# Optimization experiments

Measured on AMD Instinct MI355X. Metric: run time of the kernel, lower is better.

Reference implementation:

```python
import jax, jax.numpy as jnp
import numpy as np

B, H, W, C = 64, 56, 56, 192
NH, WS, SS = 6, 7, 3
N = WS * WS
MLP_H = 4 * C
HD = C // NH
NW = (H // WS) * (W // WS)
EPS = 1e-5


def _rel_pos_index():
    coords = np.stack(np.meshgrid(np.arange(WS), np.arange(WS), indexing='ij')).reshape(2, -1)
    rel = (coords[:, :, None] - coords[:, None, :]).transpose(1, 2, 0)
    rel[..., 0] += WS - 1
    rel[..., 1] += WS - 1
    rel[..., 0] *= 2 * WS - 1
    return rel.sum(-1)  # [N, N]


def _attn_mask():
    img = np.zeros((H, W))
    cnt = 0
    sl = (slice(0, -WS), slice(-WS, -SS), slice(-SS, None))
    for hs in sl:
        for ws in sl:
            img[hs, ws] = cnt
            cnt += 1
    mw = img.reshape(H // WS, WS, W // WS, WS).transpose(0, 2, 1, 3).reshape(-1, N)
    am = mw[:, None, :] - mw[:, :, None]
    return np.where(am != 0, -100.0, 0.0).astype(np.float32)  # [nW, N, N]


REL_IDX = jnp.asarray(_rel_pos_index())
ATTN_MASK = jnp.asarray(_attn_mask())


def _ln(x, g, b):
    m = x.mean(-1, keepdims=True)
    v = x.var(-1, keepdims=True)
    return (x - m) / jnp.sqrt(v + EPS) * g + b


def setup_inputs() -> dict:
    key = jax.random.key(0)
    ks = jax.random.split(key, 16)
    p = lambda k, shape: jax.random.normal(k, shape, dtype=jnp.float32) * 0.02
    return {
        'x': jax.random.normal(ks[0], (B, H * W, C), dtype=jnp.float32),
        'norm1_g': jnp.ones((C,), jnp.float32),
        'norm1_b': jnp.zeros((C,), jnp.float32),
        'qkv_w': p(ks[1], (3 * C, C)),
        'qkv_b': jnp.zeros((3 * C,), jnp.float32),
        'rpb': p(ks[2], ((2 * WS - 1) * (2 * WS - 1), NH)),
        'gate': jnp.full((NH,), 0.001, jnp.float32),
        'proj_w': p(ks[3], (C, C)),
        'proj_b': jnp.zeros((C,), jnp.float32),
        'norm2_g': jnp.ones((C,), jnp.float32),
        'norm2_b': jnp.zeros((C,), jnp.float32),
        'fc1_w': p(ks[4], (MLP_H, C)),
        'fc1_b': jnp.zeros((MLP_H,), jnp.float32),
        'bn_g': jnp.ones((MLP_H,), jnp.float32),
        'bn_b': jnp.zeros((MLP_H,), jnp.float32),
        'fc2_w': p(ks[5], (C, MLP_H)),
        'fc2_b': jnp.zeros((C,), jnp.float32),
    }


def reference(x, norm1_g, norm1_b, qkv_w, qkv_b, rpb, gate, proj_w, proj_b,
              norm2_g, norm2_b, fc1_w, fc1_b, bn_g, bn_b, fc2_w, fc2_b):
    shortcut = x  # [B, L, C]
    y = _ln(x, norm1_g, norm1_b).reshape(B, H, W, C)
    # cyclic shift
    y = jnp.roll(y, (-SS, -SS), axis=(1, 2))
    # window partition -> [B*nW, N, C]
    yw = y.reshape(B, H // WS, WS, W // WS, WS, C).transpose(0, 1, 3, 2, 4, 5).reshape(-1, N, C)
    qkv = (yw @ qkv_w.T + qkv_b).reshape(-1, N, 3, NH, HD).transpose(2, 0, 3, 1, 4)
    q, k, v = qkv[0], qkv[1], qkv[2]  # [B_, NH, N, HD]
    scale = HD ** (-0.5)
    attn = jnp.einsum('bhnd,bhmd->bhnm', q * scale, k)  # [B_, NH, N, N]
    bias = rpb[REL_IDX].transpose(2, 0, 1)  # [NH, N, N]
    attn = attn + bias[None]
    attn = attn.reshape(B, NW, NH, N, N) + ATTN_MASK[None, :, None]
    attn = jax.nn.softmax(attn.reshape(-1, NH, N, N), axis=-1)
    attn = attn * jax.nn.sigmoid(gate).reshape(1, NH, 1, 1)  # post-softmax gate
    o = jnp.einsum('bhnm,bhmd->bhnd', attn, v).transpose(0, 2, 1, 3).reshape(-1, N, C)
    o = o @ proj_w.T + proj_b
    # window reverse + reverse shift
    o = o.reshape(B, H // WS, W // WS, WS, WS, C).transpose(0, 1, 3, 2, 4, 5).reshape(B, H, W, C)
    o = jnp.roll(o, (SS, SS), axis=(1, 2)).reshape(B, H * W, C)
    x = shortcut + o
    # MLP with eval-mode BatchNorm1d (running_mean=0, running_var=1)
    z = _ln(x, norm2_g, norm2_b)
    z = z @ fc1_w.T + fc1_b
    z = z / jnp.sqrt(1.0 + EPS) * bn_g + bn_b
    z = jax.nn.gelu(z, approximate=False)
    z = z @ fc2_w.T + fc2_b
    return x + z
```

## Files before the change

kernel.cpp:

```cpp
#include <hip/hip_runtime.h>
#include <hip/hip_bf16.h>
#include <math.h>


typedef __attribute__((ext_vector_type(8))) short short8;
typedef __attribute__((ext_vector_type(4))) short short4v;
typedef __attribute__((ext_vector_type(4))) float floatx4;

static __device__ __forceinline__ float bf2f(__hip_bfloat16 v) { return __bfloat162float(v); }

static __device__ __forceinline__ short f2bs(float f) {
    union { __hip_bfloat16 h; short s; } u;
    u.h = __float2bfloat16(f);
    return u.s;
}

__global__ __launch_bounds__(256)
void cvt_w(const float* __restrict__ a, const float* __restrict__ b,
           const float* __restrict__ c, const float* __restrict__ d,
           __hip_bfloat16* __restrict__ o)
{
    int i = blockIdx.x * 256 + threadIdx.x;
    float v;
    if (i < 110592)      v = a[i];
    else if (i < 147456) v = b[i - 110592];
    else if (i < 294912) v = c[i - 147456];
    else                 v = d[i - 294912];
    o[i] = __float2bfloat16(v);
}

__global__ __launch_bounds__(256)
void ln1_shift_win(const float* __restrict__ x,
                   const float* __restrict__ g,
                   const float* __restrict__ bt,
                   __hip_bfloat16* __restrict__ yw)
{
    int r = blockIdx.x * 4 + (threadIdx.x >> 6);
    int lane = threadIdx.x & 63;
    int win = r / 49, t = r - win * 49;
    int b = win >> 6, wi = win & 63;
    int wh = wi >> 3, ww = wi & 7;
    int tr = t / 7, tc = t - tr * 7;
    int hs = wh * 7 + tr + 3; if (hs >= 56) hs -= 56;
    int ws = ww * 7 + tc + 3; if (ws >= 56) ws -= 56;
    const float* src = x + ((size_t)b * 3136 + hs * 56 + ws) * 192;
    float v0 = src[lane];
    float v1 = src[lane + 64];
    float v2 = src[lane + 128];
    float s  = v0 + v1 + v2;
    float s2 = v0 * v0 + v1 * v1 + v2 * v2;
#pragma unroll
    for (int off = 32; off; off >>= 1) { s += __shfl_xor(s, off); s2 += __shfl_xor(s2, off); }
    float mean = s * (1.0f / 192.0f);
    float var  = s2 * (1.0f / 192.0f) - mean * mean;
    float rstd = rsqrtf(var + 1e-5f);
    __hip_bfloat16* dst = yw + (size_t)r * 192;
    dst[lane]       = __float2bfloat16((v0 - mean) * rstd * g[lane]       + bt[lane]);
    dst[lane + 64]  = __float2bfloat16((v1 - mean) * rstd * g[lane + 64]  + bt[lane + 64]);
    dst[lane + 128] = __float2bfloat16((v2 - mean) * rstd * g[lane + 128] + bt[lane + 128]);
}

__global__ __launch_bounds__(256)
void ln2_kernel(const float* __restrict__ x1,
                const float* __restrict__ g,
                const float* __restrict__ bt,
                __hip_bfloat16* __restrict__ z)
{
    int r = blockIdx.x * 4 + (threadIdx.x >> 6);
    int lane = threadIdx.x & 63;
    const float* src = x1 + (size_t)r * 192;
    float v0 = src[lane];
    float v1 = src[lane + 64];
    float v2 = src[lane + 128];
    float s  = v0 + v1 + v2;
    float s2 = v0 * v0 + v1 * v1 + v2 * v2;
#pragma unroll
    for (int off = 32; off; off >>= 1) { s += __shfl_xor(s, off); s2 += __shfl_xor(s2, off); }
    float mean = s * (1.0f / 192.0f);
    float var  = s2 * (1.0f / 192.0f) - mean * mean;
    float rstd = rsqrtf(var + 1e-5f);
    __hip_bfloat16* dst = z + (size_t)r * 192;
    dst[lane]       = __float2bfloat16((v0 - mean) * rstd * g[lane]       + bt[lane]);
    dst[lane + 64]  = __float2bfloat16((v1 - mean) * rstd * g[lane + 64]  + bt[lane + 64]);
    dst[lane + 128] = __float2bfloat16((v2 - mean) * rstd * g[lane + 128] + bt[lane + 128]);
}

__global__ __launch_bounds__(256)
void build_tbl(const float* __restrict__ rpb, float* __restrict__ tbl)
{
    int bid = blockIdx.x;
    int head = bid >> 2, cls = bid & 3;
    int ch = cls >> 1, cw = cls & 1;
    for (int idx = threadIdx.x; idx < 4096; idx += 256) {
        int tile = idx >> 8, lane = (idx >> 2) & 63, rg = idx & 3;
        int mt = tile >> 2, nt = tile & 3;
        int lm = lane & 15, quad = lane >> 4;
        int i = nt * 16 + lm;
        int j = mt * 16 + quad * 4 + rg;
        float v;
        if (i >= 49 || j >= 49) {
            v = -1e30f;
        } else {
            int ri = i / 7, ci = i - ri * 7;
            int rj = j / 7, cj = j - rj * 7;
            int bidx = (ri - rj + 6) * 13 + (ci - cj + 6);
            v = rpb[bidx * 6 + head];
            int rio = ch ? (ri < 4 ? 1 : 2) : 0;
            int cio = cw ? (ci < 4 ? 1 : 2) : 0;
            int rjo = ch ? (rj < 4 ? 1 : 2) : 0;
            int cjo = cw ? (cj < 4 ? 1 : 2) : 0;
            if (rio * 3 + cio != rjo * 3 + cjo) v -= 100.0f;
        }
        tbl[(size_t)bid * 4096 + idx] = v;
    }
}

__global__ __launch_bounds__(256)
void attn_mfma(const __hip_bfloat16* __restrict__ qkv,
               const float* __restrict__ tbl,
               const float* __restrict__ gate,
               __hip_bfloat16* __restrict__ o)
{
    __shared__ __align__(16) char lds[49152];
    const int wave = threadIdx.x >> 6, lane = threadIdx.x & 63;
    const int lm = lane & 15, quad = lane >> 4;
    const int idx = blockIdx.x * 4 + wave;
    const int win = idx / 6;
    const int head = idx - win * 6;
    const int wi = win & 63;
    const int cls = (((wi >> 3) == 7) ? 2 : 0) + (((wi & 7) == 7) ? 1 : 0);

    char* vTb = lds + wave * 12288;
    char* Pb  = vTb + 4096;

    const __hip_bfloat16* base = qkv + (size_t)win * 49 * 576 + head * 32;

    {
        short8 v0 = {0,0,0,0,0,0,0,0}, v1 = {0,0,0,0,0,0,0,0};
        short8 v2 = {0,0,0,0,0,0,0,0}, v3 = {0,0,0,0,0,0,0,0};
        if (lane < 49) {
            const short* p = (const short*)(base + 384) + (size_t)lane * 576;
            v0 = *(const short8*)(p);
            v1 = *(const short8*)(p + 8);
            v2 = *(const short8*)(p + 16);
            v3 = *(const short8*)(p + 24);
        }
#pragma unroll
        for (int d = 0; d < 32; ++d) {
            short val = (d < 8) ? v0[d & 7] : (d < 16) ? v1[d & 7] : (d < 24) ? v2[d & 7] : v3[d & 7];
            *(short*)(vTb + ((d * 128 + lane * 2) ^ ((d & 7) << 4))) = val;
        }
    }

    short8 qf[4], kf[4];
    const short* qsrc = (const short*)base + quad * 8;
    const short* ksrc = (const short*)(base + 192) + quad * 8;
#pragma unroll
    for (int tt = 0; tt < 4; ++tt) {
        int t = tt * 16 + lm;
        if (t < 49) {
            qf[tt] = *(const short8*)(qsrc + (size_t)t * 576);
            kf[tt] = *(const short8*)(ksrc + (size_t)t * 576);
        } else {
            qf[tt] = (short8){0,0,0,0,0,0,0,0};
            kf[tt] = (short8){0,0,0,0,0,0,0,0};
        }
    }

    const floatx4 z4 = {0.f, 0.f, 0.f, 0.f};
    floatx4 s[4][4];
#pragma unroll
    for (int mt = 0; mt < 4; ++mt)
#pragma unroll
        for (int nt = 0; nt < 4; ++nt)
            s[mt][nt] = __builtin_amdgcn_mfma_f32_16x16x32_bf16(kf[mt], qf[nt], z4, 0, 0, 0);

    const float* tb = tbl + (size_t)(head * 4 + cls) * 4096 + lane * 4;
#pragma unroll
    for (int mt = 0; mt < 4; ++mt)
#pragma unroll
        for (int nt = 0; nt < 4; ++nt) {
            floatx4 b = *(const floatx4*)(tb + (mt * 4 + nt) * 256);
#pragma unroll
            for (int rg = 0; rg < 4; ++rg)
                s[mt][nt][rg] = s[mt][nt][rg] * 0.17677669529663689f + b[rg];
        }

    const float gt = 1.0f / (1.0f + __expf(-gate[head]));

    float inv[4];
#pragma unroll
    for (int nt = 0; nt < 4; ++nt) {
        float mx = -1e30f;
#pragma unroll
        for (int mt = 0; mt < 4; ++mt)
#pragma unroll
            for (int rg = 0; rg < 4; ++rg) mx = fmaxf(mx, s[mt][nt][rg]);
        mx = fmaxf(mx, __shfl_xor(mx, 16));
        mx = fmaxf(mx, __shfl_xor(mx, 32));
        float sum = 0.f;
#pragma unroll
        for (int mt = 0; mt < 4; ++mt)
#pragma unroll
            for (int rg = 0; rg < 4; ++rg) {
                float e = __expf(s[mt][nt][rg] - mx);
                s[mt][nt][rg] = e;
                sum += e;
            }
        sum += __shfl_xor(sum, 16);
        sum += __shfl_xor(sum, 32);
        inv[nt] = gt / sum;
    }

#pragma unroll
    for (int nt = 0; nt < 4; ++nt) {
        int row = nt * 16 + lm;
#pragma unroll
        for (int mt = 0; mt < 4; ++mt) {
            short4v pk = { f2bs(s[mt][nt][0] * inv[nt]), f2bs(s[mt][nt][1] * inv[nt]),
                           f2bs(s[mt][nt][2] * inv[nt]), f2bs(s[mt][nt][3] * inv[nt]) };
            int off = (row * 128 + mt * 32 + quad * 8) ^ ((row & 7) << 4);
            *(short4v*)(Pb + off) = pk;
        }
    }

    floatx4 oacc[4][2];
#pragma unroll
    for (int pt = 0; pt < 4; ++pt)
#pragma unroll
        for (int nt = 0; nt < 2; ++nt) oacc[pt][nt] = z4;

#pragma unroll
    for (int ks = 0; ks < 2; ++ks) {
        short8 vfr[2];
#pragma unroll
        for (int nt = 0; nt < 2; ++nt) {
            int row = nt * 16 + lm;
            vfr[nt] = *(const short8*)(vTb + ((row * 128 + ks * 64 + quad * 16) ^ ((row & 7) << 4)));
        }
#pragma unroll
        for (int pt = 0; pt < 4; ++pt) {
            int row = pt * 16 + lm;
            short8 pfr = *(const short8*)(Pb + ((row * 128 + ks * 64 + quad * 16) ^ ((row & 7) << 4)));
#pragma unroll
            for (int nt = 0; nt < 2; ++nt)
                oacc[pt][nt] = __builtin_amdgcn_mfma_f32_16x16x32_bf16(pfr, vfr[nt], oacc[pt][nt], 0, 0, 0);
        }
    }

    __hip_bfloat16* obase = o + (size_t)win * 49 * 192 + head * 32;
#pragma unroll
    for (int pt = 0; pt < 4; ++pt) {
#pragma unroll
        for (int rg = 0; rg < 4; ++rg) {
            int q = pt * 16 + quad * 4 + rg;
            if (q < 49) {
#pragma unroll
                for (int nt = 0; nt < 2; ++nt)
                    obase[(size_t)q * 192 + nt * 16 + lm] = __float2bfloat16(oacc[pt][nt][rg]);
            }
        }
    }
}

template <int MODE>
__global__ __launch_bounds__(256, 2)
void gemm_bt(const __hip_bfloat16* __restrict__ A,
             const __hip_bfloat16* __restrict__ W,
             const float* __restrict__ bias,
             const float* __restrict__ ex0,
             const float* __restrict__ ex1,
             void* __restrict__ OutV,
             int K, int Ncols)
{
    __shared__ __align__(16) char lds[(128 * 32 + 64 * 32) * 2];
    short* sA = (short*)lds;
    short* sB = (short*)(lds + 8192);

    const int tid  = threadIdx.x;
    const int wave = tid >> 6, lane = tid & 63;
    const int m0 = blockIdx.x * 128;
    const int n0 = blockIdx.y * 64;
    const int wm = wave >> 1, wn = wave & 1;
    const int lm = lane & 15, quad = lane >> 4;

    floatx4 acc[4][2];
#pragma unroll
    for (int mt = 0; mt < 4; ++mt)
#pragma unroll
        for (int nt = 0; nt < 2; ++nt) acc[mt][nt] = (floatx4){0.f, 0.f, 0.f, 0.f};

    for (int kk = 0; kk < K; kk += 32) {
#pragma unroll
        for (int i = 0; i < 2; ++i) {
            int c = i * 256 + tid;
            int row = c >> 2, kc = c & 3;
            const __hip_bfloat16* gp = A + (size_t)(m0 + row) * K + kk + kc * 8;
            char* lp = lds + (i * 256 + wave * 64) * 16;
            __builtin_amdgcn_global_load_lds((const __attribute__((address_space(1))) void*)gp,
                                             (__attribute__((address_space(3))) void*)lp, 16, 0, 0);
        }
        {
            int c = tid;
            int row = c >> 2, kc = c & 3;
            const __hip_bfloat16* gp = W + (size_t)(n0 + row) * K + kk + kc * 8;
            char* lp = lds + 8192 + (wave * 64) * 16;
            __builtin_amdgcn_global_load_lds((const __attribute__((address_space(1))) void*)gp,
                                             (__attribute__((address_space(3))) void*)lp, 16, 0, 0);
        }
        asm volatile("s_waitcnt vmcnt(0)" ::: "memory");
        __syncthreads();

        short8 af[4], bf[2];
#pragma unroll
        for (int mt = 0; mt < 4; ++mt)
            af[mt] = *(const short8*)(sA + ((wm * 64 + mt * 16 + lm) * 32 + quad * 8));
#pragma unroll
        for (int nt = 0; nt < 2; ++nt)
            bf[nt] = *(const short8*)(sB + ((wn * 32 + nt * 16 + lm) * 32 + quad * 8));
#pragma unroll
        for (int mt = 0; mt < 4; ++mt)
#pragma unroll
            for (int nt = 0; nt < 2; ++nt)
                acc[mt][nt] = __builtin_amdgcn_mfma_f32_16x16x32_bf16(af[mt], bf[nt], acc[mt][nt], 0, 0, 0);
        __syncthreads();
    }

#pragma unroll
    for (int mt = 0; mt < 4; ++mt) {
#pragma unroll
        for (int nt = 0; nt < 2; ++nt) {
            int col = n0 + wn * 32 + nt * 16 + lm;
            float bcol = bias[col];
#pragma unroll
            for (int rg = 0; rg < 4; ++rg) {
                int row = m0 + wm * 64 + mt * 16 + quad * 4 + rg;
                float val = acc[mt][nt][rg] + bcol;
                if (MODE == 0) {
                    ((__hip_bfloat16*)OutV)[(size_t)row * Ncols + col] = __float2bfloat16(val);
                } else if (MODE == 1) {
                    int win = row / 49, t = row - win * 49;
                    int b = win >> 6, wi = win & 63;
                    int wh = wi >> 3, ww = wi & 7;
                    int tr = t / 7, tc = t - tr * 7;
                    int h = wh * 7 + tr + 3; if (h >= 56) h -= 56;
                    int w = ww * 7 + tc + 3; if (w >= 56) w -= 56;
                    size_t dst = ((size_t)b * 3136 + h * 56 + w) * 192 + col;
                    ((float*)OutV)[dst] = val + ex0[dst];
                } else if (MODE == 2) {
                    float t2 = val * (ex0[col] * 0.99999500003749968f) + ex1[col];
                    float ge = 0.5f * t2 * (1.0f + erff(t2 * 0.70710678118654752f));
                    ((__hip_bfloat16*)OutV)[(size_t)row * Ncols + col] = __float2bfloat16(ge);
                } else {
                    size_t dst = (size_t)row * Ncols + col;
                    ((float*)OutV)[dst] = val + ex0[dst];
                }
            }
        }
    }
}

extern "C" void kernel_launch(void* const* d_in, const int* in_sizes, int n_in,
                              void* d_out, int out_size, void* d_ws, size_t ws_size,
                              hipStream_t stream)
{
    const float* x      = (const float*)d_in[0];
    const float* n1g    = (const float*)d_in[1];
    const float* n1b    = (const float*)d_in[2];
    const float* qkv_w  = (const float*)d_in[3];
    const float* qkv_b  = (const float*)d_in[4];
    const float* rpb    = (const float*)d_in[5];
    const float* gate   = (const float*)d_in[6];
    const float* proj_w = (const float*)d_in[7];
    const float* proj_b = (const float*)d_in[8];
    const float* n2g    = (const float*)d_in[9];
    const float* n2b    = (const float*)d_in[10];
    const float* fc1_w  = (const float*)d_in[11];
    const float* fc1_b  = (const float*)d_in[12];
    const float* bn_g   = (const float*)d_in[13];
    const float* bn_b   = (const float*)d_in[14];
    const float* fc2_w  = (const float*)d_in[15];
    const float* fc2_b  = (const float*)d_in[16];
    float* out = (float*)d_out;

    char* ws = (char*)d_ws;
    const int NCH = (ws_size >= 155025408u) ? 4 : 8;
    const size_t buf1max = (NCH == 4) ? 77070336u : 38535168u;
    __hip_bfloat16* buf0 = (__hip_bfloat16*)(ws);
    __hip_bfloat16* buf1 = (__hip_bfloat16*)(ws + 77070336);
    __hip_bfloat16* wbuf = (__hip_bfloat16*)(ws + 77070336 + buf1max);
    __hip_bfloat16* wq = wbuf;
    __hip_bfloat16* wp = wbuf + 110592;
    __hip_bfloat16* w1 = wbuf + 147456;
    __hip_bfloat16* w2 = wbuf + 294912;

    const int WINS = 4096 / NCH;
    const int ROWS = WINS * 49;
    const int GX   = ROWS / 128;

    float* tbl = (float*)(ws + 77070336 + (size_t)ROWS * 576 * 2);

    cvt_w<<<dim3(1728), 256, 0, stream>>>(qkv_w, proj_w, fc1_w, fc2_w, wbuf);
    build_tbl<<<dim3(24), 256, 0, stream>>>(rpb, tbl);

    ln1_shift_win<<<dim3(200704 / 4), 256, 0, stream>>>(x, n1g, n1b, buf0);

    for (int c = 0; c < NCH; ++c) {
        const __hip_bfloat16* ywc = buf0 + (size_t)c * ROWS * 192;
        __hip_bfloat16*       oc  = buf0 + (size_t)c * ROWS * 192;
        gemm_bt<0><<<dim3(GX, 9), 256, 0, stream>>>(ywc, wq, qkv_b, nullptr, nullptr, buf1, 192, 576);
        attn_mfma<<<dim3(WINS * 6 / 4), 256, 0, stream>>>(buf1, tbl, gate, oc);
    }

    gemm_bt<1><<<dim3(1568, 3), 256, 0, stream>>>(buf0, wp, proj_b, x, nullptr, out, 192, 192);

    ln2_kernel<<<dim3(200704 / 4), 256, 0, stream>>>(out, n2g, n2b, buf0);

    for (int c = 0; c < NCH; ++c) {
        const __hip_bfloat16* zc = buf0 + (size_t)c * ROWS * 192;
        float*                xc = out  + (size_t)c * ROWS * 192;
        gemm_bt<2><<<dim3(GX, 12), 256, 0, stream>>>(zc, w1, fc1_b, bn_g, bn_b, buf1, 192, 768);
        gemm_bt<3><<<dim3(GX, 3), 256, 0, stream>>>(buf1, w2, fc2_b, xc, nullptr, xc, 768, 192);
    }
}
```

Measured before the change: 965.5 us.

## Fuse LayerNorm2, fc1+BN+GELU and fc2 into one MLP kernel

Replaces the ln2 kernel and the chunked fc1/fc2 GEMM launches with a single kernel per 64-row tile. The tile is normalized into LDS, and the 768-wide hidden layer is produced 128 columns at a time into double-buffered LDS, then consumed immediately by fc2 with register accumulators. The aim is to stop writing and re-reading the large hidden activation and the normalized input through global memory, and to cut launch count. In exchange, each block reloads weight fragments straight from global memory without LDS staging, and register pressure is high, which may limit occupancy.

```diff
diff --git a/kernel.cpp b/kernel.cpp
--- a/kernel.cpp
+++ b/kernel.cpp
@@ -55,31 +55,6 @@
     float var  = s2 * (1.0f / 192.0f) - mean * mean;
     float rstd = rsqrtf(var + 1e-5f);
     __hip_bfloat16* dst = yw + (size_t)r * 192;
-    dst[lane]       = __float2bfloat16((v0 - mean) * rstd * g[lane]       + bt[lane]);
-    dst[lane + 64]  = __float2bfloat16((v1 - mean) * rstd * g[lane + 64]  + bt[lane + 64]);
-    dst[lane + 128] = __float2bfloat16((v2 - mean) * rstd * g[lane + 128] + bt[lane + 128]);
-}
-
-__global__ __launch_bounds__(256)
-void ln2_kernel(const float* __restrict__ x1,
-                const float* __restrict__ g,
-                const float* __restrict__ bt,
-                __hip_bfloat16* __restrict__ z)
-{
-    int r = blockIdx.x * 4 + (threadIdx.x >> 6);
-    int lane = threadIdx.x & 63;
-    const float* src = x1 + (size_t)r * 192;
-    float v0 = src[lane];
-    float v1 = src[lane + 64];
-    float v2 = src[lane + 128];
-    float s  = v0 + v1 + v2;
-    float s2 = v0 * v0 + v1 * v1 + v2 * v2;
-#pragma unroll
-    for (int off = 32; off; off >>= 1) { s += __shfl_xor(s, off); s2 += __shfl_xor(s2, off); }
-    float mean = s * (1.0f / 192.0f);
-    float var  = s2 * (1.0f / 192.0f) - mean * mean;
-    float rstd = rsqrtf(var + 1e-5f);
-    __hip_bfloat16* dst = z + (size_t)r * 192;
     dst[lane]       = __float2bfloat16((v0 - mean) * rstd * g[lane]       + bt[lane]);
     dst[lane + 64]  = __float2bfloat16((v1 - mean) * rstd * g[lane + 64]  + bt[lane + 64]);
     dst[lane + 128] = __float2bfloat16((v2 - mean) * rstd * g[lane + 128] + bt[lane + 128]);
@@ -338,7 +313,7 @@
                 float val = acc[mt][nt][rg] + bcol;
                 if (MODE == 0) {
                     ((__hip_bfloat16*)OutV)[(size_t)row * Ncols + col] = __float2bfloat16(val);
-                } else if (MODE == 1) {
+                } else {
                     int win = row / 49, t = row - win * 49;
                     int b = win >> 6, wi = win & 63;
                     int wh = wi >> 3, ww = wi & 7;
@@ -347,14 +322,148 @@
                     int w = ww * 7 + tc + 3; if (w >= 56) w -= 56;
                     size_t dst = ((size_t)b * 3136 + h * 56 + w) * 192 + col;
                     ((float*)OutV)[dst] = val + ex0[dst];
-                } else if (MODE == 2) {
-                    float t2 = val * (ex0[col] * 0.99999500003749968f) + ex1[col];
+                }
+            }
+        }
+    }
+}
+
+__global__ __launch_bounds__(256, 2)
+void mlp_fused(float* __restrict__ xio,
+               const __hip_bfloat16* __restrict__ w1,
+               const __hip_bfloat16* __restrict__ w2,
+               const float* __restrict__ fc1_b,
+               const float* __restrict__ bn_g,
+               const float* __restrict__ bn_b,
+               const float* __restrict__ fc2_b,
+               const float* __restrict__ n2g,
+               const float* __restrict__ n2b)
+{
+    constexpr int ZS = 200;
+    constexpr int HS = 136;
+    __shared__ __align__(16) short zbuf[64 * ZS];
+    __shared__ __align__(16) short hbuf[2][64 * HS];
+
+    const int tid = threadIdx.x;
+    const int wave = tid >> 6, lane = tid & 63;
+    const int lm = lane & 15, quad = lane >> 4;
+    const int wm = wave >> 1, wn = wave & 1;
+    const int m0 = blockIdx.x * 64;
+
+    {
+        float g0 = n2g[lane], g1 = n2g[lane + 64], g2 = n2g[lane + 128];
+        float b0 = n2b[lane], b1 = n2b[lane + 64], b2 = n2b[lane + 128];
+        for (int rr = 0; rr < 16; ++rr) {
+            int row = wave * 16 + rr;
+            const float* src = xio + (size_t)(m0 + row) * 192;
+            float v0 = src[lane], v1 = src[lane + 64], v2 = src[lane + 128];
+            float s = v0 + v1 + v2;
+            float s2 = v0 * v0 + v1 * v1 + v2 * v2;
+#pragma unroll
+            for (int off = 32; off; off >>= 1) { s += __shfl_xor(s, off); s2 += __shfl_xor(s2, off); }
+            float mean = s * (1.0f / 192.0f);
+            float var  = s2 * (1.0f / 192.0f) - mean * mean;
+            float rstd = rsqrtf(var + 1e-5f);
+            zbuf[row * ZS + lane]       = f2bs((v0 - mean) * rstd * g0 + b0);
+            zbuf[row * ZS + lane + 64]  = f2bs((v1 - mean) * rstd * g1 + b1);
+            zbuf[row * ZS + lane + 128] = f2bs((v2 - mean) * rstd * g2 + b2);
+        }
+    }
+    __syncthreads();
+
+    floatx4 acc[2][6];
+#pragma unroll
+    for (int mt = 0; mt < 2; ++mt)
+#pragma unroll
+        for (int nt = 0; nt < 6; ++nt) acc[mt][nt] = (floatx4){0.f, 0.f, 0.f, 0.f};
+
+    const short* w1s = (const short*)w1;
+    const short* w2s = (const short*)w2;
+
+    auto phaseA = [&](int s, int buf) {
+        floatx4 a2[4][2];
+#pragma unroll
+        for (int nt = 0; nt < 4; ++nt)
+#pragma unroll
+            for (int mt = 0; mt < 2; ++mt) a2[nt][mt] = (floatx4){0.f, 0.f, 0.f, 0.f};
+#pragma unroll
+        for (int ks = 0; ks < 6; ++ks) {
+            short8 zf[2], wf[4];
+#pragma unroll
+            for (int mt = 0; mt < 2; ++mt)
+                zf[mt] = *(const short8*)(zbuf + (wm * 32 + mt * 16 + lm) * ZS + ks * 32 + quad * 8);
+#pragma unroll
+            for (int nt = 0; nt < 4; ++nt)
+                wf[nt] = *(const short8*)(w1s + (size_t)(s * 128 + wn * 64 + nt * 16 + lm) * 192 + ks * 32 + quad * 8);
+#pragma unroll
+            for (int nt = 0; nt < 4; ++nt)
+#pragma unroll
+                for (int mt = 0; mt < 2; ++mt)
+                    a2[nt][mt] = __builtin_amdgcn_mfma_f32_16x16x32_bf16(wf[nt], zf[mt], a2[nt][mt], 0, 0, 0);
+        }
+        short* hb = &hbuf[0][0] + buf * (64 * HS);
+#pragma unroll
+        for (int nt = 0; nt < 4; ++nt) {
+            int colb = s * 128 + wn * 64 + nt * 16 + quad * 4;
+            float fb[4], G[4], B2[4];
+#pragma unroll
+            for (int rg = 0; rg < 4; ++rg) {
+                fb[rg] = fc1_b[colb + rg];
+                G[rg]  = bn_g[colb + rg] * 0.99999500003749968f;
+                B2[rg] = bn_b[colb + rg];
+            }
+#pragma unroll
+            for (int mt = 0; mt < 2; ++mt) {
+                int row = wm * 32 + mt * 16 + lm;
+                short4v pk;
+#pragma unroll
+                for (int rg = 0; rg < 4; ++rg) {
+                    float t2 = (a2[nt][mt][rg] + fb[rg]) * G[rg] + B2[rg];
                     float ge = 0.5f * t2 * (1.0f + erff(t2 * 0.70710678118654752f));
-                    ((__hip_bfloat16*)OutV)[(size_t)row * Ncols + col] = __float2bfloat16(ge);
-                } else {
-                    size_t dst = (size_t)row * Ncols + col;
-                    ((float*)OutV)[dst] = val + ex0[dst];
+                    pk[rg] = f2bs(ge);
                 }
+                *(short4v*)(hb + row * HS + wn * 64 + nt * 16 + quad * 4) = pk;
+            }
+        }
+    };
+
+    auto phaseB = [&](int s, int buf) {
+        const short* hb = &hbuf[0][0] + buf * (64 * HS);
+#pragma unroll
+        for (int ks = 0; ks < 4; ++ks) {
+            short8 hf[2], vf[6];
+#pragma unroll
+            for (int mt = 0; mt < 2; ++mt)
+                hf[mt] = *(const short8*)(hb + (wm * 32 + mt * 16 + lm) * HS + ks * 32 + quad * 8);
+#pragma unroll
+            for (int nt = 0; nt < 6; ++nt)
+                vf[nt] = *(const short8*)(w2s + (size_t)(wn * 96 + nt * 16 + lm) * 768 + s * 128 + ks * 32 + quad * 8);
+#pragma unroll
+            for (int mt = 0; mt < 2; ++mt)
+#pragma unroll
+                for (int nt = 0; nt < 6; ++nt)
+                    acc[mt][nt] = __builtin_amdgcn_mfma_f32_16x16x32_bf16(hf[mt], vf[nt], acc[mt][nt], 0, 0, 0);
+        }
+    };
+
+    phaseA(0, 0);
+    __syncthreads();
+    for (int s = 0; s < 6; ++s) {
+        if (s < 5) phaseA(s + 1, (s + 1) & 1);
+        phaseB(s, s & 1);
+        __syncthreads();
+    }
+
+#pragma unroll
+    for (int mt = 0; mt < 2; ++mt) {
+#pragma unroll
+        for (int nt = 0; nt < 6; ++nt) {
+            int col = wn * 96 + nt * 16 + lm;
+            float fb = fc2_b[col];
+#pragma unroll
+            for (int rg = 0; rg < 4; ++rg) {
+                size_t dst = (size_t)(m0 + wm * 32 + mt * 16 + quad * 4 + rg) * 192 + col;
+                xio[dst] = acc[mt][nt][rg] + fb + xio[dst];
             }
         }
     }
@@ -414,12 +523,5 @@
 
     gemm_bt<1><<<dim3(1568, 3), 256, 0, stream>>>(buf0, wp, proj_b, x, nullptr, out, 192, 192);
 
-    ln2_kernel<<<dim3(200704 / 4), 256, 0, stream>>>(out, n2g, n2b, buf0);
-
-    for (int c = 0; c < NCH; ++c) {
-        const __hip_bfloat16* zc = buf0 + (size_t)c * ROWS * 192;
-        float*                xc = out  + (size_t)c * ROWS * 192;
-        gemm_bt<2><<<dim3(GX, 12), 256, 0, stream>>>(zc, w1, fc1_b, bn_g, bn_b, buf1, 192, 768);
-        gemm_bt<3><<<dim3(GX, 3), 256, 0, stream>>>(buf1, w2, fc2_b, xc, nullptr, xc, 768, 192);
-    }
-}
+    mlp_fused<<<dim3(3136), 256, 0, stream>>>(out, w1, w2, fc1_b, bn_g, bn_b, fc2_b, n2g, n2b);
+}
```

New measurement: 1.150 ms. 1.19x slower.
